# Performance work log

Hardware: AMD Instinct MI355X
Metric: run time of the kernel (lower is better)

## Reference

```python
import jax, jax.numpy as jnp
import numpy as np

B, S, H = 2, 2048, 1024          # batch, seq, hidden_size
I = 512                          # expert_ffn_hidden_size
E_R, E_Z = 32, 8                 # routed experts, zero (identity) experts
E_T = E_R + E_Z                  # total experts
K = 6                            # moe_topk
SCALE = 2.5                      # routed_scaling_factor
W_INIT = 0.02


def setup_inputs() -> dict:
    key = jax.random.key(0)
    k0, k1, k2, k3 = jax.random.split(key, 4)
    return {
        "hidden_states": jax.random.normal(k0, (B, S, H), jnp.float32),
        "classifier_weight": jax.random.normal(k1, (E_T, H), jnp.float32) * W_INIT,
        "e_score_correction_bias": jnp.zeros((E_T,), jnp.float32),
        "gate_up_proj": jax.random.normal(k2, (E_T, 2 * I, H), jnp.float32) * W_INIT,
        "down_proj": jax.random.normal(k3, (E_R, H, I), jnp.float32) * W_INIT,
    }


def reference(hidden_states, classifier_weight, e_score_correction_bias,
              gate_up_proj, down_proj):
    orig_shape = hidden_states.shape
    x = hidden_states.reshape(-1, H).astype(jnp.float32)      # [T, H]
    T = x.shape[0]

    # ---- router (fp32 like the torch code) ----
    logits = x @ classifier_weight.T                          # [T, E_T]
    scores = jax.nn.softmax(logits, axis=-1)
    _, topk_idx = jax.lax.top_k(scores + e_score_correction_bias[None, :], K)
    topk_w = jnp.take_along_axis(scores, topk_idx, axis=1) * SCALE  # [T, K]

    # dense per-(token, expert) combine weights; 0 for unselected experts
    w_full = jnp.zeros((T, E_T), jnp.float32).at[
        jnp.arange(T)[:, None], topk_idx].add(topk_w)          # [T, E_T]

    # zero experts: weighted identity
    zero_w = w_full[:, E_R:].sum(axis=-1, keepdims=True)       # [T, 1]
    out0 = x * zero_w

    # routed experts: SwiGLU MLP per expert, scanned over experts
    routed_w = w_full[:, :E_R].T                               # [E_R, T]

    def body(out, xs):
        Wgu, Wd, we = xs                                       # [2I,H],[H,I],[T]
        gate, up = jnp.split(x @ Wgu.T, 2, axis=-1)            # [T, I] each
        y = (jax.nn.silu(gate) * up) @ Wd.T                    # [T, H]
        return out + we[:, None] * y, None

    out, _ = jax.lax.scan(body, out0, (gate_up_proj[:E_R], down_proj, routed_w))
    return out.reshape(orig_shape).astype(hidden_states.dtype)
```

## Files before the change

kernel.cpp:

```cpp
#include <hip/hip_runtime.h>
#include <float.h>
#include <math.h>

#define TT 4096
#define HH 1024
#define II 512
#define E_R 32
#define E_T 40
#define TOPK 6
#define SCALE_F 2.5f
#define MAXTILES 224

typedef __bf16 bf16x8 __attribute__((ext_vector_type(8)));
typedef float f32x4 __attribute__((ext_vector_type(4)));

__device__ inline unsigned short f2bf(float f) {
  __bf16 h = (__bf16)f;
  return __builtin_bit_cast(unsigned short, h);
}

__device__ inline uint4 cvt8(float4 a, float4 b) {
  bf16x8 v;
  v[0] = (__bf16)a.x; v[1] = (__bf16)a.y; v[2] = (__bf16)a.z; v[3] = (__bf16)a.w;
  v[4] = (__bf16)b.x; v[5] = (__bf16)b.y; v[6] = (__bf16)b.z; v[7] = (__bf16)b.w;
  return __builtin_bit_cast(uint4, v);
}

__device__ inline void gload_lds16(const void* g, void* l) {
  __builtin_amdgcn_global_load_lds(
      (__attribute__((address_space(1))) void*)g,
      (__attribute__((address_space(3))) void*)l, 16, 0, 0);
}

__device__ inline void lds_store16(unsigned short* base, int row, int c8, uint4 v) {
  int byte = (row * 128 + c8 * 16) ^ ((row & 7) << 4);
  *reinterpret_cast<uint4*>(reinterpret_cast<char*>(base) + byte) = v;
}
__device__ inline bf16x8 lds_frag(const unsigned short* base, int row, int kb) {
  int byte = (row * 128 + kb * 2) ^ ((row & 7) << 4);
  uint4 v = *reinterpret_cast<const uint4*>(reinterpret_cast<const char*>(base) + byte);
  return __builtin_bit_cast(bf16x8, v);
}

__device__ inline f32x4 mfma16(bf16x8 a, bf16x8 b, f32x4 c) {
  return __builtin_amdgcn_mfma_f32_16x16x32_bf16(a, b, c, 0, 0, 0);
}

__global__ __launch_bounds__(256) void k_logits(const float* __restrict__ x,
                                                const float* __restrict__ wcls,
                                                float* __restrict__ logits,
                                                unsigned short* __restrict__ xb) {
  __shared__ float4 ws4[E_T * 64];
  const int tid = threadIdx.x;
  const int lane = tid & 63;
  const int wave = tid >> 6;
  const int token = blockIdx.x * 4 + wave;
  const float4* x4 = reinterpret_cast<const float4*>(x);
  const float4* w4 = reinterpret_cast<const float4*>(wcls);

  float acc[E_T];
  #pragma unroll
  for (int e = 0; e < E_T; ++e) acc[e] = 0.f;

  for (int c = 0; c < 4; ++c) {
    if (c) __syncthreads();
    #pragma unroll
    for (int j = 0; j < 10; ++j) {
      int v = tid + j * 256;
      int e = v >> 6, kq = v & 63;
      ws4[v] = w4[e * 256 + c * 64 + kq];
    }
    float4 xv = x4[(size_t)token * 256 + c * 64 + lane];
    ushort4 s;
    s.x = f2bf(xv.x); s.y = f2bf(xv.y); s.z = f2bf(xv.z); s.w = f2bf(xv.w);
    reinterpret_cast<ushort4*>(xb + (size_t)token * HH)[c * 64 + lane] = s;
    __syncthreads();
    #pragma unroll
    for (int e = 0; e < E_T; ++e) {
      float4 w = ws4[e * 64 + lane];
      acc[e] += xv.x * w.x + xv.y * w.y + xv.z * w.z + xv.w * w.w;
    }
  }

  float mine = 0.f;
  #pragma unroll
  for (int e = 0; e < E_T; ++e) {
    float r = acc[e];
    #pragma unroll
    for (int o = 32; o; o >>= 1) r += __shfl_xor(r, o);
    if (lane == e) mine = r;
  }
  if (lane < E_T) logits[(size_t)token * E_T + lane] = mine;
}

__global__ void k_topk(const float* __restrict__ logits, const float* __restrict__ bias,
                       float* __restrict__ zero_w, int* __restrict__ counts,
                       int* __restrict__ tok_list,
                       int* __restrict__ route_ep, float* __restrict__ route_w,
                       int* __restrict__ route_n) {
  int t = blockIdx.x * 64 + threadIdx.x;
  float l[E_T];
  const float4* lp = reinterpret_cast<const float4*>(logits + (size_t)t * E_T);
  #pragma unroll
  for (int j = 0; j < E_T / 4; ++j) {
    float4 v = lp[j];
    l[j * 4 + 0] = v.x; l[j * 4 + 1] = v.y; l[j * 4 + 2] = v.z; l[j * 4 + 3] = v.w;
  }
  float m = -FLT_MAX;
  #pragma unroll
  for (int e = 0; e < E_T; ++e) m = fmaxf(m, l[e]);
  float den = 0.f;
  #pragma unroll
  for (int e = 0; e < E_T; ++e) { l[e] = __expf(l[e] - m); den += l[e]; }
  float inv = 1.f / den;
  float sel[E_T];
  #pragma unroll
  for (int e = 0; e < E_T; ++e) { l[e] *= inv; sel[e] = l[e] + bias[e]; }

  unsigned long long used = 0ull;
  float zw = 0.f;
  int nr = 0;
  for (int k = 0; k < TOPK; ++k) {
    float bv = -FLT_MAX; int bj = 0;
    #pragma unroll
    for (int e = 0; e < E_T; ++e) {
      float v = ((used >> e) & 1ull) ? -FLT_MAX : sel[e];
      if (v > bv) { bv = v; bj = e; }
    }
    used |= 1ull << bj;
    float wgt = (bv - bias[bj]) * SCALE_F;
    if (bj >= E_R) {
      zw += wgt;
    } else {
      int p = atomicAdd(&counts[bj], 1);
      tok_list[bj * TT + p] = t;
      route_ep[t * TOPK + nr] = (bj << 16) | p;
      route_w[t * TOPK + nr] = wgt;
      nr++;
    }
  }
  zero_w[t] = zw;
  route_n[t] = nr;
}

__global__ void k_scan(const int* __restrict__ counts, int* __restrict__ offsets,
                       int* __restrict__ tiles) {
  if (threadIdx.x == 0) {
    int s = 0, idx = 0;
    for (int e = 0; e < E_R; ++e) {
      offsets[e] = s;
      int c = counts[e];
      s += c;
      for (int r0 = 0; r0 < c; r0 += 128) tiles[1 + idx++] = (e << 16) | r0;
    }
    offsets[E_R] = s;
    tiles[0] = idx;
  }
}

__global__ __launch_bounds__(256, 4) void k_gemm1(
    const unsigned short* __restrict__ xb, const float* __restrict__ gup,
    const int* __restrict__ tok_list, const int* __restrict__ counts,
    const int* __restrict__ offsets, const int* __restrict__ tiles,
    unsigned short* __restrict__ inter) {
  const int nt = tiles[0];
  if ((int)blockIdx.y >= nt) return;
  const int tv = tiles[1 + blockIdx.y];
  const int e = tv >> 16;
  const int row0 = tv & 0xffff;
  const int cnt = counts[e];
  const int off = offsets[e];
  const int n0 = blockIdx.x * 64;
  const int tid = threadIdx.x;
  const int lane = tid & 63;
  const int wave = tid >> 6;
  const int wr = wave >> 1;
  const int wc = wave & 1;

  __shared__ __align__(16) unsigned short lA[128 * 64];
  __shared__ __align__(16) unsigned short lBg[64 * 64];
  __shared__ __align__(16) unsigned short lBu[64 * 64];
  __shared__ int toks[128];

  if (tid < 128) {
    int r = row0 + tid;
    toks[tid] = tok_list[e * TT + (r < cnt ? r : cnt - 1)];
  }
  __syncthreads();

  unsigned aoff[4];
  #pragma unroll
  for (int i = 0; i < 4; ++i) {
    int lrow = wave * 32 + i * 8 + (lane >> 3);
    aoff[i] = (unsigned)toks[lrow] * HH + (((lane & 7) ^ (lrow & 7)) * 8);
  }
  const float4* g4 = reinterpret_cast<const float4*>(gup + (size_t)e * 1024 * HH);
  unsigned boff[2];
  int brow[2], bc8[2];
  #pragma unroll
  for (int s = 0; s < 2; ++s) {
    int idx = tid + s * 256;
    brow[s] = idx >> 3; bc8[s] = idx & 7;
    boff[s] = (unsigned)(n0 + brow[s]) * (HH / 4) + bc8[s] * 2;
  }
  const unsigned upjump = 512u * (HH / 4);

  f32x4 accg[4][2] = {}; f32x4 accu[4][2] = {};

  for (int k0 = 0; k0 < HH; k0 += 64) {
    unsigned kq = k0 >> 2;
    #pragma unroll
    for (int i = 0; i < 4; ++i)
      gload_lds16(xb + aoff[i] + k0, lA + (wave * 32 + i * 8) * 64);
    #pragma unroll
    for (int s = 0; s < 2; ++s) {
      float4 ga = g4[boff[s] + kq], gb = g4[boff[s] + kq + 1];
      lds_store16(lBg, brow[s], bc8[s], cvt8(ga, gb));
      float4 ua = g4[boff[s] + upjump + kq], ub = g4[boff[s] + upjump + kq + 1];
      lds_store16(lBu, brow[s], bc8[s], cvt8(ua, ub));
    }
    __syncthreads();
    #pragma unroll
    for (int ks = 0; ks < 2; ++ks) {
      int kb = ks * 32 + ((lane >> 4) << 3);
      bf16x8 a[4], g[2], u[2];
      #pragma unroll
      for (int i = 0; i < 4; ++i) a[i] = lds_frag(lA, wr * 64 + i * 16 + (lane & 15), kb);
      #pragma unroll
      for (int j = 0; j < 2; ++j) {
        g[j] = lds_frag(lBg, wc * 32 + j * 16 + (lane & 15), kb);
        u[j] = lds_frag(lBu, wc * 32 + j * 16 + (lane & 15), kb);
      }
      #pragma unroll
      for (int i = 0; i < 4; ++i)
        #pragma unroll
        for (int j = 0; j < 2; ++j) {
          accg[i][j] = mfma16(a[i], g[j], accg[i][j]);
          accu[i][j] = mfma16(a[i], u[j], accu[i][j]);
        }
    }
    __syncthreads();
  }

  #pragma unroll
  for (int i = 0; i < 4; ++i)
    #pragma unroll
    for (int j = 0; j < 2; ++j)
      #pragma unroll
      for (int r = 0; r < 4; ++r) {
        int rloc = wr * 64 + i * 16 + ((lane >> 4) << 2) + r;
        int grow = row0 + rloc;
        if (grow < cnt) {
          int col = n0 + wc * 32 + j * 16 + (lane & 15);
          float gv = accg[i][j][r], uv = accu[i][j][r];
          float act = gv / (1.f + __expf(-gv)) * uv;
          inter[(size_t)(off + grow) * II + col] = f2bf(act);
        }
      }
}

__global__ __launch_bounds__(256, 4) void k_gemm2(
    const unsigned short* __restrict__ inter, const float* __restrict__ dwn,
    const int* __restrict__ counts, const int* __restrict__ offsets,
    const int* __restrict__ tiles, unsigned short* __restrict__ inter2) {
  const int nt = tiles[0];
  if ((int)blockIdx.y >= nt) return;
  const int tv = tiles[1 + blockIdx.y];
  const int e = tv >> 16;
  const int row0 = tv & 0xffff;
  const int cnt = counts[e];
  const int off = offsets[e];
  const int h0 = blockIdx.x * 128;
  const int tid = threadIdx.x;
  const int lane = tid & 63;
  const int wave = tid >> 6;
  const int wr = wave >> 1;
  const int wc = wave & 1;

  __shared__ __align__(16) unsigned short lA[128 * 64];
  __shared__ __align__(16) unsigned short lB[128 * 64];

  unsigned aoff[4];
  #pragma unroll
  for (int i = 0; i < 4; ++i) {
    int lrow = wave * 32 + i * 8 + (lane >> 3);
    int rr = row0 + lrow; rr = rr < cnt ? rr : cnt - 1;
    aoff[i] = (unsigned)(off + rr) * II + (((lane & 7) ^ (lrow & 7)) * 8);
  }
  const float4* d4 = reinterpret_cast<const float4*>(dwn + (size_t)e * HH * II);
  unsigned boff[4];
  int brow[4], bc8[4];
  #pragma unroll
  for (int s = 0; s < 4; ++s) {
    int idx = tid + s * 256;
    brow[s] = idx >> 3; bc8[s] = idx & 7;
    boff[s] = (unsigned)(h0 + brow[s]) * (II / 4) + bc8[s] * 2;
  }

  f32x4 acc[4][4] = {};

  for (int k0 = 0; k0 < II; k0 += 64) {
    unsigned kq = k0 >> 2;
    #pragma unroll
    for (int i = 0; i < 4; ++i)
      gload_lds16(inter + aoff[i] + k0, lA + (wave * 32 + i * 8) * 64);
    #pragma unroll
    for (int s = 0; s < 4; ++s) {
      float4 a = d4[boff[s] + kq], b = d4[boff[s] + kq + 1];
      lds_store16(lB, brow[s], bc8[s], cvt8(a, b));
    }
    __syncthreads();
    #pragma unroll
    for (int ks = 0; ks < 2; ++ks) {
      int kb = ks * 32 + ((lane >> 4) << 3);
      bf16x8 a[4], b[4];
      #pragma unroll
      for (int i = 0; i < 4; ++i) a[i] = lds_frag(lA, wr * 64 + i * 16 + (lane & 15), kb);
      #pragma unroll
      for (int j = 0; j < 4; ++j) b[j] = lds_frag(lB, wc * 64 + j * 16 + (lane & 15), kb);
      #pragma unroll
      for (int i = 0; i < 4; ++i)
        #pragma unroll
        for (int j = 0; j < 4; ++j)
          acc[i][j] = mfma16(a[i], b[j], acc[i][j]);
    }
    __syncthreads();
  }

  #pragma unroll
  for (int i = 0; i < 4; ++i)
    #pragma unroll
    for (int j = 0; j < 4; ++j)
      #pragma unroll
      for (int r = 0; r < 4; ++r) {
        int rloc = wr * 64 + i * 16 + ((lane >> 4) << 2) + r;
        int grow = row0 + rloc;
        if (grow < cnt) {
          int h = h0 + wc * 64 + j * 16 + (lane & 15);
          inter2[(size_t)(off + grow) * HH + h] = f2bf(acc[i][j][r]);
        }
      }
}

__global__ __launch_bounds__(256) void k_combine(
    const float* __restrict__ x, const float* __restrict__ zero_w,
    const int* __restrict__ offsets, const int* __restrict__ route_ep,
    const float* __restrict__ route_w, const int* __restrict__ route_n,
    const unsigned short* __restrict__ inter2, float* __restrict__ out) {
  const int t = blockIdx.x;
  const int tid = threadIdx.x;
  const float zw = zero_w[t];
  const int n = route_n[t];
  float4 o = reinterpret_cast<const float4*>(x)[t * 256 + tid];
  o.x *= zw; o.y *= zw; o.z *= zw; o.w *= zw;
  for (int i = 0; i < n; ++i) {
    int ep = route_ep[t * TOPK + i];
    int row = offsets[ep >> 16] + (ep & 0xffff);
    float w = route_w[t * TOPK + i];
    ushort4 v = reinterpret_cast<const ushort4*>(inter2 + (size_t)row * HH)[tid];
    o.x += w * __builtin_bit_cast(float, (unsigned)v.x << 16);
    o.y += w * __builtin_bit_cast(float, (unsigned)v.y << 16);
    o.z += w * __builtin_bit_cast(float, (unsigned)v.z << 16);
    o.w += w * __builtin_bit_cast(float, (unsigned)v.w << 16);
  }
  reinterpret_cast<float4*>(out)[t * 256 + tid] = o;
}


extern "C" void kernel_launch(void* const* d_in, const int* in_sizes, int n_in,
                              void* d_out, int out_size, void* d_ws, size_t ws_size,
                              hipStream_t stream) {
  const float* x    = (const float*)d_in[0];
  const float* wcls = (const float*)d_in[1];
  const float* bias = (const float*)d_in[2];
  const float* gup  = (const float*)d_in[3];
  const float* dwn  = (const float*)d_in[4];
  float* out = (float*)d_out;

  char* w = (char*)d_ws;
  unsigned short* xb    = (unsigned short*)(w + 0);
  float* zero_w         = (float*)(w + 8388608);
  int* counts           = (int*)(w + 8404992);
  int* offsets          = (int*)(w + 8405120);
  int* tok_list         = (int*)(w + 8405376);
  float* logits         = (float*)(w + 8929664);
  int* tiles            = (int*)(w + 9585024);
  int* route_ep         = (int*)(w + 9589120);
  float* route_w        = (float*)(w + 9687424);
  int* route_n          = (int*)(w + 9785728);
  unsigned short* inter = (unsigned short*)(w + 9802112);
  unsigned short* inter2 = (unsigned short*)(w + 34967936);

  hipMemsetAsync(counts, 0, E_R * sizeof(int), stream);
  k_logits<<<1024, 256, 0, stream>>>(x, wcls, logits, xb);
  k_topk<<<64, 64, 0, stream>>>(logits, bias, zero_w, counts, tok_list,
                                route_ep, route_w, route_n);
  k_scan<<<1, 64, 0, stream>>>(counts, offsets, tiles);
  k_gemm1<<<dim3(8, MAXTILES), 256, 0, stream>>>(xb, gup, tok_list, counts, offsets, tiles, inter);
  k_gemm2<<<dim3(8, MAXTILES), 256, 0, stream>>>(inter, dwn, counts, offsets, tiles, inter2);
  k_combine<<<TT, 256, 0, stream>>>(x, zero_w, offsets, route_ep, route_w, route_n,
                                    inter2, out);
}
```

Before: 262.7 us.

## Stage fp32 expert weights into LDS via direct loads, convert to bf16 at fragment read

```diff
diff --git a/kernel.cpp b/kernel.cpp
--- a/kernel.cpp
+++ b/kernel.cpp
@@ -19,11 +19,11 @@
   return __builtin_bit_cast(unsigned short, h);
 }
 
-__device__ inline uint4 cvt8(float4 a, float4 b) {
+__device__ inline bf16x8 cvt8v(float4 a, float4 b) {
   bf16x8 v;
   v[0] = (__bf16)a.x; v[1] = (__bf16)a.y; v[2] = (__bf16)a.z; v[3] = (__bf16)a.w;
   v[4] = (__bf16)b.x; v[5] = (__bf16)b.y; v[6] = (__bf16)b.z; v[7] = (__bf16)b.w;
-  return __builtin_bit_cast(uint4, v);
+  return v;
 }
 
 __device__ inline void gload_lds16(const void* g, void* l) {
@@ -32,14 +32,20 @@
       (__attribute__((address_space(3))) void*)l, 16, 0, 0);
 }
 
-__device__ inline void lds_store16(unsigned short* base, int row, int c8, uint4 v) {
-  int byte = (row * 128 + c8 * 16) ^ ((row & 7) << 4);
-  *reinterpret_cast<uint4*>(reinterpret_cast<char*>(base) + byte) = v;
-}
 __device__ inline bf16x8 lds_frag(const unsigned short* base, int row, int kb) {
   int byte = (row * 128 + kb * 2) ^ ((row & 7) << 4);
   uint4 v = *reinterpret_cast<const uint4*>(reinterpret_cast<const char*>(base) + byte);
   return __builtin_bit_cast(bf16x8, v);
+}
+
+__device__ inline bf16x8 lds_frag_f32(const float* base, int row, int kb) {
+  int key = row & 15;
+  int c0 = (kb >> 2) ^ key;
+  int c1 = ((kb >> 2) + 1) ^ key;
+  const char* p = reinterpret_cast<const char*>(base) + row * 256;
+  float4 lo = *reinterpret_cast<const float4*>(p + c0 * 16);
+  float4 hi = *reinterpret_cast<const float4*>(p + c1 * 16);
+  return cvt8v(lo, hi);
 }
 
 __device__ inline f32x4 mfma16(bf16x8 a, bf16x8 b, f32x4 c) {
@@ -158,7 +164,7 @@
   }
 }
 
-__global__ __launch_bounds__(256, 4) void k_gemm1(
+__global__ __launch_bounds__(256, 3) void k_gemm1(
     const unsigned short* __restrict__ xb, const float* __restrict__ gup,
     const int* __restrict__ tok_list, const int* __restrict__ counts,
     const int* __restrict__ offsets, const int* __restrict__ tiles,
@@ -178,8 +184,8 @@
   const int wc = wave & 1;
 
   __shared__ __align__(16) unsigned short lA[128 * 64];
-  __shared__ __align__(16) unsigned short lBg[64 * 64];
-  __shared__ __align__(16) unsigned short lBu[64 * 64];
+  __shared__ __align__(16) float lBg[64 * 64];
+  __shared__ __align__(16) float lBu[64 * 64];
   __shared__ int toks[128];
 
   if (tid < 128) {
@@ -194,30 +200,25 @@
     int lrow = wave * 32 + i * 8 + (lane >> 3);
     aoff[i] = (unsigned)toks[lrow] * HH + (((lane & 7) ^ (lrow & 7)) * 8);
   }
-  const float4* g4 = reinterpret_cast<const float4*>(gup + (size_t)e * 1024 * HH);
-  unsigned boff[2];
-  int brow[2], bc8[2];
-  #pragma unroll
-  for (int s = 0; s < 2; ++s) {
-    int idx = tid + s * 256;
-    brow[s] = idx >> 3; bc8[s] = idx & 7;
-    boff[s] = (unsigned)(n0 + brow[s]) * (HH / 4) + bc8[s] * 2;
-  }
-  const unsigned upjump = 512u * (HH / 4);
+  const float* gbase = gup + (size_t)e * 1024 * HH;
+  unsigned boff[4];
+  #pragma unroll
+  for (int i = 0; i < 4; ++i) {
+    int rt = wave * 16 + i * 4 + (lane >> 4);
+    boff[i] = (unsigned)(n0 + rt) * HH + (((lane & 15) ^ (rt & 15)) * 4);
+  }
+  const unsigned upjump = 512u * HH;
 
   f32x4 accg[4][2] = {}; f32x4 accu[4][2] = {};
 
   for (int k0 = 0; k0 < HH; k0 += 64) {
-    unsigned kq = k0 >> 2;
     #pragma unroll
     for (int i = 0; i < 4; ++i)
       gload_lds16(xb + aoff[i] + k0, lA + (wave * 32 + i * 8) * 64);
     #pragma unroll
-    for (int s = 0; s < 2; ++s) {
-      float4 ga = g4[boff[s] + kq], gb = g4[boff[s] + kq + 1];
-      lds_store16(lBg, brow[s], bc8[s], cvt8(ga, gb));
-      float4 ua = g4[boff[s] + upjump + kq], ub = g4[boff[s] + upjump + kq + 1];
-      lds_store16(lBu, brow[s], bc8[s], cvt8(ua, ub));
+    for (int i = 0; i < 4; ++i) {
+      gload_lds16(gbase + boff[i] + k0,          lBg + (wave * 16 + i * 4) * 64);
+      gload_lds16(gbase + boff[i] + upjump + k0, lBu + (wave * 16 + i * 4) * 64);
     }
     __syncthreads();
     #pragma unroll
@@ -228,8 +229,8 @@
       for (int i = 0; i < 4; ++i) a[i] = lds_frag(lA, wr * 64 + i * 16 + (lane & 15), kb);
       #pragma unroll
       for (int j = 0; j < 2; ++j) {
-        g[j] = lds_frag(lBg, wc * 32 + j * 16 + (lane & 15), kb);
-        u[j] = lds_frag(lBu, wc * 32 + j * 16 + (lane & 15), kb);
+        g[j] = lds_frag_f32(lBg, wc * 32 + j * 16 + (lane & 15), kb);
+        u[j] = lds_frag_f32(lBu, wc * 32 + j * 16 + (lane & 15), kb);
       }
       #pragma unroll
       for (int i = 0; i < 4; ++i)
@@ -259,7 +260,7 @@
       }
 }
 
-__global__ __launch_bounds__(256, 4) void k_gemm2(
+__global__ __launch_bounds__(256, 3) void k_gemm2(
     const unsigned short* __restrict__ inter, const float* __restrict__ dwn,
     const int* __restrict__ counts, const int* __restrict__ offsets,
     const int* __restrict__ tiles, unsigned short* __restrict__ inter2) {
@@ -278,7 +279,7 @@
   const int wc = wave & 1;
 
   __shared__ __align__(16) unsigned short lA[128 * 64];
-  __shared__ __align__(16) unsigned short lB[128 * 64];
+  __shared__ __align__(16) float lB[128 * 64];
 
   unsigned aoff[4];
   #pragma unroll
@@ -287,28 +288,23 @@
     int rr = row0 + lrow; rr = rr < cnt ? rr : cnt - 1;
     aoff[i] = (unsigned)(off + rr) * II + (((lane & 7) ^ (lrow & 7)) * 8);
   }
-  const float4* d4 = reinterpret_cast<const float4*>(dwn + (size_t)e * HH * II);
-  unsigned boff[4];
-  int brow[4], bc8[4];
-  #pragma unroll
-  for (int s = 0; s < 4; ++s) {
-    int idx = tid + s * 256;
-    brow[s] = idx >> 3; bc8[s] = idx & 7;
-    boff[s] = (unsigned)(h0 + brow[s]) * (II / 4) + bc8[s] * 2;
+  const float* dbase = dwn + (size_t)e * HH * II;
+  unsigned boff[8];
+  #pragma unroll
+  for (int i = 0; i < 8; ++i) {
+    int rt = wave * 32 + i * 4 + (lane >> 4);
+    boff[i] = (unsigned)(h0 + rt) * II + (((lane & 15) ^ (rt & 15)) * 4);
   }
 
   f32x4 acc[4][4] = {};
 
   for (int k0 = 0; k0 < II; k0 += 64) {
-    unsigned kq = k0 >> 2;
     #pragma unroll
     for (int i = 0; i < 4; ++i)
       gload_lds16(inter + aoff[i] + k0, lA + (wave * 32 + i * 8) * 64);
     #pragma unroll
-    for (int s = 0; s < 4; ++s) {
-      float4 a = d4[boff[s] + kq], b = d4[boff[s] + kq + 1];
-      lds_store16(lB, brow[s], bc8[s], cvt8(a, b));
-    }
+    for (int i = 0; i < 8; ++i)
+      gload_lds16(dbase + boff[i] + k0, lB + (wave * 32 + i * 4) * 64);
     __syncthreads();
     #pragma unroll
     for (int ks = 0; ks < 2; ++ks) {
@@ -317,7 +313,7 @@
       #pragma unroll
       for (int i = 0; i < 4; ++i) a[i] = lds_frag(lA, wr * 64 + i * 16 + (lane & 15), kb);
       #pragma unroll
-      for (int j = 0; j < 4; ++j) b[j] = lds_frag(lB, wc * 64 + j * 16 + (lane & 15), kb);
+      for (int j = 0; j < 4; ++j) b[j] = lds_frag_f32(lB, wc * 64 + j * 16 + (lane & 15), kb);
       #pragma unroll
       for (int i = 0; i < 4; ++i)
         #pragma unroll
```

New measurement: 227.3 us. -13.4%, faster.
